# Performance work log

Hardware: AMD Instinct MI355X
Metric: run time of the kernel (lower is better)

The kernel has to match this reference:

```python
import jax, jax.numpy as jnp
import numpy as np

N, D, NUM_CLASSES = 4096, 512, 128
MARGIN = 0.3


def setup_inputs() -> dict:
    key = jax.random.key(0)
    k1, k2 = jax.random.split(key)
    embeddings = jax.random.normal(k1, (N, D), dtype=jnp.float32)
    labels = jax.random.randint(k2, (N,), 0, NUM_CLASSES, dtype=jnp.int64)
    return {"embeddings": embeddings, "labels": labels}


def _batch_hard_triplet(embeddings, labels, margin):
    # L2-normalize rows (torch F.normalize: x / max(||x||, eps))
    norm = jnp.linalg.norm(embeddings, axis=1, keepdims=True)
    e = embeddings / jnp.maximum(norm, 1e-12)
    n = e.shape[0]
    # Pairwise Euclidean distance via Gram matrix; ||a-b||^2 = 2 - 2 a.b for unit vectors
    gram = e @ e.T                                   # [N, N]
    sq = jnp.clip(2.0 - 2.0 * gram, 0.0, None)
    # safe sqrt: zero (and exactly-equal) pairs get distance 0 with zero gradient
    nz = sq > 0
    dist = jnp.where(nz, jnp.sqrt(jnp.where(nz, sq, 1.0)), 0.0)  # [N, N]

    same = labels[:, None] == labels[None, :]        # [N, N] bool
    eye = jnp.eye(n, dtype=bool)
    pos_mask = same & ~eye                           # positives excluding self
    neg_mask = ~same

    # hardest positive (row max over positives), hardest negative (row min over negatives)
    dist_ap = jnp.max(jnp.where(pos_mask, dist, -jnp.inf), axis=1)  # [N]
    dist_an = jnp.min(jnp.where(neg_mask, dist, jnp.inf), axis=1)   # [N]

    valid = jnp.any(pos_mask, axis=1) & jnp.any(neg_mask, axis=1)   # rows kept by torch loop
    per_row = jax.nn.relu(dist_ap - dist_an + margin)
    num_valid = jnp.sum(valid)
    loss_sum = jnp.sum(jnp.where(valid, per_row, 0.0))
    return jnp.where(num_valid > 0, loss_sum / jnp.maximum(num_valid, 1), 0.0)


def reference(embeddings, labels):
    return _batch_hard_triplet(embeddings, labels, MARGIN)
```

## Files before the change

kernel.cpp:

```cpp
#include <hip/hip_runtime.h>
#include <hip/hip_bf16.h>
#include <stdint.h>


#define NROW 4096
#define DIM  512
#define MARGIN 0.3f
#define BT 128
#define BK 32
#define NTILE (NROW / BT)
#define NPAIR (NTILE * (NTILE + 1) / 2)
#define POS_INIT 0xFFFFFFFFu
#define NEG_INIT 0u

typedef __attribute__((ext_vector_type(8))) __bf16 bf16x8;
typedef __attribute__((ext_vector_type(4))) float  f32x4;

__device__ __forceinline__ unsigned enc(float f) {
    unsigned u = __float_as_uint(f);
    return (u & 0x80000000u) ? ~u : (u | 0x80000000u);
}
__device__ __forceinline__ float dec(unsigned e) {
    return (e & 0x80000000u) ? __uint_as_float(e & 0x7fffffffu)
                             : __uint_as_float(~e);
}

__device__ __forceinline__ unsigned short f2bf(float f) {
    __hip_bfloat16 h = __float2bfloat16(f);
    return *reinterpret_cast<unsigned short*>(&h);
}

__device__ __forceinline__ void async_copy16(const void* g, void* l) {
    __builtin_amdgcn_global_load_lds(
        (const __attribute__((address_space(1))) unsigned int*)g,
        (__attribute__((address_space(3))) unsigned int*)l,
        16, 0, 0);
}

__global__ void tl_norm(const float* __restrict__ E,
                        __hip_bfloat16* __restrict__ Ebf,
                        unsigned* __restrict__ posArr,
                        unsigned* __restrict__ negArr) {
    if (blockIdx.x < 16) {
        int t = blockIdx.x * 256 + threadIdx.x;
        posArr[t] = POS_INIT;
        negArr[t] = NEG_INIT;
    }
    int wave = threadIdx.x >> 6;
    int lane = threadIdx.x & 63;
    int row  = blockIdx.x * 4 + wave;

    const float4* src = (const float4*)(E + (size_t)row * DIM);
    float4 v0 = src[lane];
    float4 v1 = src[lane + 64];
    float ss = v0.x*v0.x + v0.y*v0.y + v0.z*v0.z + v0.w*v0.w
             + v1.x*v1.x + v1.y*v1.y + v1.z*v1.z + v1.w*v1.w;
    #pragma unroll
    for (int m = 32; m >= 1; m >>= 1) ss += __shfl_xor(ss, m);
    float inv = 1.0f / fmaxf(sqrtf(ss), 1e-12f);

    ushort4 o0, o1;
    o0.x = f2bf(v0.x * inv); o0.y = f2bf(v0.y * inv);
    o0.z = f2bf(v0.z * inv); o0.w = f2bf(v0.w * inv);
    o1.x = f2bf(v1.x * inv); o1.y = f2bf(v1.y * inv);
    o1.z = f2bf(v1.z * inv); o1.w = f2bf(v1.w * inv);
    ushort4* dst = (ushort4*)(Ebf + (size_t)row * DIM);
    dst[lane]      = o0;
    dst[lane + 64] = o1;
}

__global__ void tl_gram(const __hip_bfloat16* __restrict__ Ebf,
                        const int* __restrict__ labels,
                        unsigned* __restrict__ posArr,
                        unsigned* __restrict__ negArr) {
    __shared__ __align__(16) __hip_bfloat16 At[BT * BK];
    __shared__ __align__(16) __hip_bfloat16 Bt[BT * BK];
    __shared__ int rowLab[BT];
    __shared__ int colLab[BT];

    int t = blockIdx.x, bi = 0, rowlen = NTILE;
    while (t >= rowlen) { t -= rowlen; rowlen--; bi++; }
    const int bj = bi + t;

    const int tid  = threadIdx.x;
    const int wave = tid >> 6;
    const int lane = tid & 63;
    const int quad = lane >> 4;
    const int l16  = lane & 15;
    const int wr   = wave >> 1;
    const int wc   = wave & 1;
    const int tileI = bi * BT;
    const int tileJ = bj * BT;
    const bool diag = (bi == bj);

    if (tid < BT) rowLab[tid] = labels[tileI + tid];
    else          colLab[tid - BT] = labels[tileJ + (tid - BT)];

    const int sRow = wave * 32 + (lane >> 2);
    const int sK   = (lane & 3) * 8;
    const __hip_bfloat16* gA = Ebf + (size_t)(tileI + sRow) * DIM + sK;
    const __hip_bfloat16* gB = Ebf + (size_t)(tileJ + sRow) * DIM + sK;
    __hip_bfloat16* lA0 = &At[(wave * 2 + 0) * 512];
    __hip_bfloat16* lA1 = &At[(wave * 2 + 1) * 512];
    __hip_bfloat16* lB0 = &Bt[(wave * 2 + 0) * 512];
    __hip_bfloat16* lB1 = &Bt[(wave * 2 + 1) * 512];

    f32x4 acc[4][4] = {};

    for (int k0 = 0; k0 < DIM; k0 += BK) {
        async_copy16(gA + k0,            lA0);
        async_copy16(gA + k0 + 16 * DIM, lA1);
        async_copy16(gB + k0,            lB0);
        async_copy16(gB + k0 + 16 * DIM, lB1);
        __syncthreads();

        bf16x8 a[4], b[4];
        #pragma unroll
        for (int mi = 0; mi < 4; mi++)
            a[mi] = *(const bf16x8*)&At[(wr * 64 + mi * 16 + l16) * BK + quad * 8];
        #pragma unroll
        for (int ni = 0; ni < 4; ni++)
            b[ni] = *(const bf16x8*)&Bt[(wc * 64 + ni * 16 + l16) * BK + quad * 8];

        #pragma unroll
        for (int mi = 0; mi < 4; mi++)
            #pragma unroll
            for (int ni = 0; ni < 4; ni++)
                acc[mi][ni] = __builtin_amdgcn_mfma_f32_16x16x32_bf16(
                    a[mi], b[ni], acc[mi][ni], 0, 0, 0);

        __syncthreads();
    }

    int rl[16], cl[4], clocv[4];
    #pragma unroll
    for (int mi = 0; mi < 4; mi++)
        #pragma unroll
        for (int reg = 0; reg < 4; reg++)
            rl[mi * 4 + reg] = rowLab[wr * 64 + mi * 16 + quad * 4 + reg];
    #pragma unroll
    for (int ni = 0; ni < 4; ni++) {
        clocv[ni] = wc * 64 + ni * 16 + l16;
        cl[ni] = colLab[clocv[ni]];
    }

    #pragma unroll
    for (int mi = 0; mi < 4; mi++) {
        #pragma unroll
        for (int reg = 0; reg < 4; reg++) {
            const int rloc = wr * 64 + mi * 16 + quad * 4 + reg;
            const int lr   = rl[mi * 4 + reg];
            const int gi   = tileI + rloc;
            float pmin =  INFINITY;
            float nmax = -INFINITY;
            #pragma unroll
            for (int ni = 0; ni < 4; ni++) {
                const int gj  = tileJ + clocv[ni];
                const float g = acc[mi][ni][reg];
                const bool same = (lr == cl[ni]);
                if (same && gi != gj) pmin = fminf(pmin, g);
                if (!same)            nmax = fmaxf(nmax, g);
            }
            #pragma unroll
            for (int m = 1; m < 16; m <<= 1) {
                pmin = fminf(pmin, __shfl_xor(pmin, m));
                nmax = fmaxf(nmax, __shfl_xor(nmax, m));
            }
            if (l16 == 0) {
                if (pmin <  INFINITY) atomicMin(&posArr[gi], enc(pmin));
                if (nmax > -INFINITY) atomicMax(&negArr[gi], enc(nmax));
            }
        }
    }

    if (!diag) {
        #pragma unroll
        for (int ni = 0; ni < 4; ni++) {
            const int lc = cl[ni];
            const int gj = tileJ + clocv[ni];
            float pmin =  INFINITY;
            float nmax = -INFINITY;
            #pragma unroll
            for (int mi = 0; mi < 4; mi++) {
                #pragma unroll
                for (int reg = 0; reg < 4; reg++) {
                    const float g = acc[mi][ni][reg];
                    const bool same = (rl[mi * 4 + reg] == lc);
                    if (same) pmin = fminf(pmin, g);
                    else      nmax = fmaxf(nmax, g);
                }
            }
            pmin = fminf(pmin, __shfl_xor(pmin, 16));
            pmin = fminf(pmin, __shfl_xor(pmin, 32));
            nmax = fmaxf(nmax, __shfl_xor(nmax, 16));
            nmax = fmaxf(nmax, __shfl_xor(nmax, 32));
            if (quad == 0) {
                if (pmin <  INFINITY) atomicMin(&posArr[gj], enc(pmin));
                if (nmax > -INFINITY) atomicMax(&negArr[gj], enc(nmax));
            }
        }
    }
}

__global__ void tl_final(const unsigned* __restrict__ posArr,
                         const unsigned* __restrict__ negArr,
                         float* __restrict__ out) {
    const int tid = threadIdx.x;
    float sum = 0.0f;
    int   count = 0;
    for (int i = tid; i < NROW; i += 256) {
        const unsigned pe = posArr[i];
        const unsigned ne = negArr[i];
        const bool valid = (pe != POS_INIT) && (ne != NEG_INIT);
        const float dap = sqrtf(fmaxf(2.0f - 2.0f * dec(pe), 0.0f));
        const float dan = sqrtf(fmaxf(2.0f - 2.0f * dec(ne), 0.0f));
        const float per = fmaxf(dap - dan + MARGIN, 0.0f);
        if (valid) { sum += per; count += 1; }
    }
    #pragma unroll
    for (int m = 32; m >= 1; m >>= 1) {
        sum   += __shfl_xor(sum, m);
        count += __shfl_xor(count, m);
    }
    __shared__ float ssum[4];
    __shared__ int   scnt[4];
    const int wave = tid >> 6, lane = tid & 63;
    if (lane == 0) { ssum[wave] = sum; scnt[wave] = count; }
    __syncthreads();
    if (tid == 0) {
        float s = ssum[0] + ssum[1] + ssum[2] + ssum[3];
        int   c = scnt[0] + scnt[1] + scnt[2] + scnt[3];
        out[0] = (c > 0) ? (s / (float)c) : 0.0f;
    }
}

extern "C" void kernel_launch(void* const* d_in, const int* in_sizes, int n_in,
                              void* d_out, int out_size, void* d_ws, size_t ws_size,
                              hipStream_t stream) {
    const float* E      = (const float*)d_in[0];
    const int*   labels = (const int*)d_in[1];
    float*       out    = (float*)d_out;

    char* ws = (char*)d_ws;
    __hip_bfloat16* Ebf   = (__hip_bfloat16*)ws;
    unsigned* posArr      = (unsigned*)(ws + (size_t)NROW * DIM * 2);
    unsigned* negArr      = posArr + NROW;

    tl_norm<<<NROW / 4, 256, 0, stream>>>(E, Ebf, posArr, negArr);
    tl_gram<<<NPAIR, 256, 0, stream>>>(Ebf, labels, posArr, negArr);
    tl_final<<<1, 256, 0, stream>>>(posArr, negArr, out);
}
```

Baseline: 92.73 us.

## Load MFMA fragments directly from global with register double-buffering

The Gram kernel no longer stages A/B tiles through LDS with barriers on every K step. Each wave now loads its bf16 MFMA fragments straight from global memory into registers, double-buffered so the next K slice is prefetched while the current MFMAs run. This removes the barriers and LDS traffic, at the cost of duplicated global/L1 loads across waves and higher register pressure. The normalization kernel also writes one 16-byte vector per lane, and the final reduction uses 1024 threads with one vector load each instead of a strided loop.

After: 116.3 us. 1.25x slower.

```diff
diff --git a/kernel.cpp b/kernel.cpp
--- a/kernel.cpp
+++ b/kernel.cpp
@@ -7,7 +7,6 @@
 #define DIM  512
 #define MARGIN 0.3f
 #define BT 128
-#define BK 32
 #define NTILE (NROW / BT)
 #define NPAIR (NTILE * (NTILE + 1) / 2)
 #define POS_INIT 0xFFFFFFFFu
@@ -15,6 +14,7 @@
 
 typedef __attribute__((ext_vector_type(8))) __bf16 bf16x8;
 typedef __attribute__((ext_vector_type(4))) float  f32x4;
+typedef __attribute__((ext_vector_type(8))) unsigned short u16x8;
 
 __device__ __forceinline__ unsigned enc(float f) {
     unsigned u = __float_as_uint(f);
@@ -28,13 +28,6 @@
 __device__ __forceinline__ unsigned short f2bf(float f) {
     __hip_bfloat16 h = __float2bfloat16(f);
     return *reinterpret_cast<unsigned short*>(&h);
-}
-
-__device__ __forceinline__ void async_copy16(const void* g, void* l) {
-    __builtin_amdgcn_global_load_lds(
-        (const __attribute__((address_space(1))) unsigned int*)g,
-        (__attribute__((address_space(3))) unsigned int*)l,
-        16, 0, 0);
 }
 
 __global__ void tl_norm(const float* __restrict__ E,
@@ -51,30 +44,26 @@
     int row  = blockIdx.x * 4 + wave;
 
     const float4* src = (const float4*)(E + (size_t)row * DIM);
-    float4 v0 = src[lane];
-    float4 v1 = src[lane + 64];
+    float4 v0 = src[2 * lane];
+    float4 v1 = src[2 * lane + 1];
     float ss = v0.x*v0.x + v0.y*v0.y + v0.z*v0.z + v0.w*v0.w
              + v1.x*v1.x + v1.y*v1.y + v1.z*v1.z + v1.w*v1.w;
     #pragma unroll
     for (int m = 32; m >= 1; m >>= 1) ss += __shfl_xor(ss, m);
     float inv = 1.0f / fmaxf(sqrtf(ss), 1e-12f);
 
-    ushort4 o0, o1;
-    o0.x = f2bf(v0.x * inv); o0.y = f2bf(v0.y * inv);
-    o0.z = f2bf(v0.z * inv); o0.w = f2bf(v0.w * inv);
-    o1.x = f2bf(v1.x * inv); o1.y = f2bf(v1.y * inv);
-    o1.z = f2bf(v1.z * inv); o1.w = f2bf(v1.w * inv);
-    ushort4* dst = (ushort4*)(Ebf + (size_t)row * DIM);
-    dst[lane]      = o0;
-    dst[lane + 64] = o1;
+    u16x8 o;
+    o[0] = f2bf(v0.x * inv); o[1] = f2bf(v0.y * inv);
+    o[2] = f2bf(v0.z * inv); o[3] = f2bf(v0.w * inv);
+    o[4] = f2bf(v1.x * inv); o[5] = f2bf(v1.y * inv);
+    o[6] = f2bf(v1.z * inv); o[7] = f2bf(v1.w * inv);
+    ((u16x8*)(Ebf + (size_t)row * DIM))[lane] = o;
 }
 
 __global__ void tl_gram(const __hip_bfloat16* __restrict__ Ebf,
                         const int* __restrict__ labels,
                         unsigned* __restrict__ posArr,
                         unsigned* __restrict__ negArr) {
-    __shared__ __align__(16) __hip_bfloat16 At[BT * BK];
-    __shared__ __align__(16) __hip_bfloat16 Bt[BT * BK];
     __shared__ int rowLab[BT];
     __shared__ int colLab[BT];
 
@@ -95,41 +84,35 @@
 
     if (tid < BT) rowLab[tid] = labels[tileI + tid];
     else          colLab[tid - BT] = labels[tileJ + (tid - BT)];
-
-    const int sRow = wave * 32 + (lane >> 2);
-    const int sK   = (lane & 3) * 8;
-    const __hip_bfloat16* gA = Ebf + (size_t)(tileI + sRow) * DIM + sK;
-    const __hip_bfloat16* gB = Ebf + (size_t)(tileJ + sRow) * DIM + sK;
-    __hip_bfloat16* lA0 = &At[(wave * 2 + 0) * 512];
-    __hip_bfloat16* lA1 = &At[(wave * 2 + 1) * 512];
-    __hip_bfloat16* lB0 = &Bt[(wave * 2 + 0) * 512];
-    __hip_bfloat16* lB1 = &Bt[(wave * 2 + 1) * 512];
+    __syncthreads();
+
+    const __hip_bfloat16* pA = Ebf + (size_t)(tileI + wr * 64 + l16) * DIM + quad * 8;
+    const __hip_bfloat16* pB = Ebf + (size_t)(tileJ + wc * 64 + l16) * DIM + quad * 8;
 
     f32x4 acc[4][4] = {};
-
-    for (int k0 = 0; k0 < DIM; k0 += BK) {
-        async_copy16(gA + k0,            lA0);
-        async_copy16(gA + k0 + 16 * DIM, lA1);
-        async_copy16(gB + k0,            lB0);
-        async_copy16(gB + k0 + 16 * DIM, lB1);
-        __syncthreads();
-
-        bf16x8 a[4], b[4];
-        #pragma unroll
-        for (int mi = 0; mi < 4; mi++)
-            a[mi] = *(const bf16x8*)&At[(wr * 64 + mi * 16 + l16) * BK + quad * 8];
-        #pragma unroll
-        for (int ni = 0; ni < 4; ni++)
-            b[ni] = *(const bf16x8*)&Bt[(wc * 64 + ni * 16 + l16) * BK + quad * 8];
-
+    bf16x8 a[2][4], b[2][4];
+
+    #pragma unroll
+    for (int i = 0; i < 4; i++) {
+        a[0][i] = *(const bf16x8*)(pA + i * 16 * DIM);
+        b[0][i] = *(const bf16x8*)(pB + i * 16 * DIM);
+    }
+    #pragma unroll
+    for (int kk = 0; kk < 16; ++kk) {
+        const int cur = kk & 1, nxt = cur ^ 1;
+        if (kk < 15) {
+            #pragma unroll
+            for (int i = 0; i < 4; i++) {
+                a[nxt][i] = *(const bf16x8*)(pA + i * 16 * DIM + (kk + 1) * 32);
+                b[nxt][i] = *(const bf16x8*)(pB + i * 16 * DIM + (kk + 1) * 32);
+            }
+        }
         #pragma unroll
         for (int mi = 0; mi < 4; mi++)
             #pragma unroll
             for (int ni = 0; ni < 4; ni++)
                 acc[mi][ni] = __builtin_amdgcn_mfma_f32_16x16x32_bf16(
-                    a[mi], b[ni], acc[mi][ni], 0, 0, 0);
-
-        __syncthreads();
+                    a[cur][mi], b[cur][ni], acc[mi][ni], 0, 0, 0);
     }
 
     int rl[16], cl[4], clocv[4];
@@ -206,14 +189,17 @@
                          const unsigned* __restrict__ negArr,
                          float* __restrict__ out) {
     const int tid = threadIdx.x;
+    uint4 pe4 = ((const uint4*)posArr)[tid];
+    uint4 ne4 = ((const uint4*)negArr)[tid];
+    unsigned pes[4] = {pe4.x, pe4.y, pe4.z, pe4.w};
+    unsigned nes[4] = {ne4.x, ne4.y, ne4.z, ne4.w};
     float sum = 0.0f;
     int   count = 0;
-    for (int i = tid; i < NROW; i += 256) {
-        const unsigned pe = posArr[i];
-        const unsigned ne = negArr[i];
-        const bool valid = (pe != POS_INIT) && (ne != NEG_INIT);
-        const float dap = sqrtf(fmaxf(2.0f - 2.0f * dec(pe), 0.0f));
-        const float dan = sqrtf(fmaxf(2.0f - 2.0f * dec(ne), 0.0f));
+    #pragma unroll
+    for (int j = 0; j < 4; j++) {
+        const bool valid = (pes[j] != POS_INIT) && (nes[j] != NEG_INIT);
+        const float dap = sqrtf(fmaxf(2.0f - 2.0f * dec(pes[j]), 0.0f));
+        const float dan = sqrtf(fmaxf(2.0f - 2.0f * dec(nes[j]), 0.0f));
         const float per = fmaxf(dap - dan + MARGIN, 0.0f);
         if (valid) { sum += per; count += 1; }
     }
@@ -222,14 +208,15 @@
         sum   += __shfl_xor(sum, m);
         count += __shfl_xor(count, m);
     }
-    __shared__ float ssum[4];
-    __shared__ int   scnt[4];
+    __shared__ float ssum[16];
+    __shared__ int   scnt[16];
     const int wave = tid >> 6, lane = tid & 63;
     if (lane == 0) { ssum[wave] = sum; scnt[wave] = count; }
     __syncthreads();
     if (tid == 0) {
-        float s = ssum[0] + ssum[1] + ssum[2] + ssum[3];
-        int   c = scnt[0] + scnt[1] + scnt[2] + scnt[3];
+        float s = 0.0f; int c = 0;
+        #pragma unroll
+        for (int w = 0; w < 16; w++) { s += ssum[w]; c += scnt[w]; }
         out[0] = (c > 0) ? (s / (float)c) : 0.0f;
     }
 }
@@ -248,5 +235,5 @@
 
     tl_norm<<<NROW / 4, 256, 0, stream>>>(E, Ebf, posArr, negArr);
     tl_gram<<<NPAIR, 256, 0, stream>>>(Ebf, labels, posArr, negArr);
-    tl_final<<<1, 256, 0, stream>>>(posArr, negArr, out);
-}
+    tl_final<<<1, 1024, 0, stream>>>(posArr, negArr, out);
+}
```
